# Optimization experiments

Measured on AMD Instinct MI355X. Metric: run time of the kernel, lower is better.

The kernel has to match this reference:

```python
import jax, jax.numpy as jnp
import numpy as np

N_NODES = 50000
N_EDGES = 600000
D = 128
EPS = 1e-5
AVG_D_LOG = float(np.log(4 + 1))  # avg_d={'log': log(avg_d+1)}, avg_d=4


def setup_inputs() -> dict:
    key = jax.random.key(0)
    ks = jax.random.split(key, 8)
    h = jax.random.normal(ks[0], (N_NODES, D), dtype=jnp.float32)
    # guarantee every node has at least one incoming edge (self-loop)
    edge_dst = jnp.concatenate([
        jnp.arange(N_NODES, dtype=jnp.int64),
        jax.random.randint(ks[1], (N_EDGES - N_NODES,), 0, N_NODES).astype(jnp.int64),
    ])
    edge_src = jax.random.randint(ks[2], (N_EDGES,), 0, N_NODES).astype(jnp.int64)
    def lin(k, fan_in, fan_out):
        lim = 1.0 / np.sqrt(fan_in)
        return jax.random.uniform(k, (fan_in, fan_out), jnp.float32, -lim, lim)
    W_pre = lin(ks[3], 2 * D, D)
    b_pre = jnp.zeros((D,), jnp.float32)
    W_post = lin(ks[4], 12 * D + D, D)  # 4 aggregators * 3 scalers * D + in_dim
    b_post = jnp.zeros((D,), jnp.float32)
    W_mix = lin(ks[5], D, D)
    b_mix = jnp.zeros((D,), jnp.float32)
    return {"h": h, "edge_src": edge_src, "edge_dst": edge_dst,
            "W_pre": W_pre, "b_pre": b_pre, "W_post": W_post,
            "b_post": b_post, "W_mix": W_mix, "b_mix": b_mix}


def reference(h, edge_src, edge_dst, W_pre, b_pre, W_post, b_post, W_mix, b_mix):
    n = h.shape[0]
    # pretrans_edges: cat(src, dst) -> Linear -> ReLU (MLP act) -> ReLU (outer)
    z2 = jnp.concatenate([h[edge_src], h[edge_dst]], axis=1)        # [E, 2D]
    e = jax.nn.relu(z2 @ W_pre + b_pre)                             # [E, D]
    # multi-aggregator segment reduce over destination nodes
    deg = jax.ops.segment_sum(jnp.ones_like(edge_dst, jnp.float32), edge_dst, n)  # [N]
    inv_deg = 1.0 / deg[:, None]
    mean = jax.ops.segment_sum(e, edge_dst, n) * inv_deg
    mean_sq = jax.ops.segment_sum(e * e, edge_dst, n) * inv_deg
    std = jnp.sqrt(jax.nn.relu(mean_sq - mean * mean) + EPS)
    mx = jax.ops.segment_max(e, edge_dst, n)
    mn = jax.ops.segment_min(e, edge_dst, n)
    agg = jnp.concatenate([mean, mx, mn, std], axis=1)              # [N, 4D]
    # scalers: identity, amplification, attenuation
    log_d = jnp.log(deg + 1.0)[:, None]
    scaled = jnp.concatenate([agg, agg * (log_d / AVG_D_LOG), agg * (AVG_D_LOG / log_d)], axis=1)  # [N, 12D]
    # posttrans: cat(h, aggregated) -> Linear -> ReLU
    hp = jax.nn.relu(jnp.concatenate([h, scaled], axis=1) @ W_post + b_post)  # [N, D]
    # mixing network + residual (node_dim == out_dim)
    out = h + jax.nn.leaky_relu(hp @ W_mix + b_mix, negative_slope=0.01)
    return out
```

## Files before the change

### kernel.cpp

```cpp
#include <hip/hip_runtime.h>
#include <hip/hip_bf16.h>

#define N_NODES 50000
#define N_EDGES 600000
#define D 128

constexpr float AVG_D_LOG = 1.6094379124341003f;
constexpr float EPS_V = 1e-5f;

#define PQ_B     0ul
#define AGG_B    25600000ul
#define HBF_B    76800000ul
#define WPRET2_B 89600000ul
#define WPOSTT_B 89665536ul
#define WMIXT_B  90091520ul
#define DEGC_B   90124288ul
#define OFF_B    90324288ul
#define CUR_B    90524352ul
#define SRCS_B   90724352ul
#define GCNT_B   93124352ul

typedef __attribute__((ext_vector_type(8))) short bf16x8;
typedef __attribute__((ext_vector_type(4))) float f32x4;

__device__ __forceinline__ short f2b(float f) {
    unsigned u = __builtin_bit_cast(unsigned, f);
    u += 0x7fffu + ((u >> 16) & 1u);
    return (short)(u >> 16);
}
__device__ __forceinline__ unsigned pk2(float a, float b) {
    return (unsigned)(unsigned short)f2b(a) | ((unsigned)(unsigned short)f2b(b) << 16);
}
__device__ __forceinline__ float blo(unsigned u) { return __uint_as_float(u << 16); }
__device__ __forceinline__ float bhi(unsigned u) { return __uint_as_float(u & 0xffff0000u); }

__device__ __forceinline__ void gld_lds16(const void* g, void* l) {
    __builtin_amdgcn_global_load_lds(
        (const __attribute__((address_space(1))) void*)g,
        (__attribute__((address_space(3))) void*)l, 16, 0, 0);
}

#define WAIT_BAR(N) do {                                              \
    asm volatile("s_waitcnt vmcnt(" #N ")" ::: "memory");             \
    __builtin_amdgcn_sched_barrier(0);                                \
    __builtin_amdgcn_s_barrier();                                     \
    __builtin_amdgcn_sched_barrier(0);                                \
} while (0)
#define BAR_ONLY() do {                                               \
    __builtin_amdgcn_sched_barrier(0);                                \
    __builtin_amdgcn_s_barrier();                                     \
    __builtin_amdgcn_sched_barrier(0);                                \
} while (0)

__global__ __launch_bounds__(256) void prep_kernel(
    const float* __restrict__ h, const float* __restrict__ Wpre,
    const float* __restrict__ Wpost, const float* __restrict__ Wmix,
    short* __restrict__ hbf, short* __restrict__ wpreT2,
    short* __restrict__ wpostT, short* __restrict__ wmixT,
    int* __restrict__ degc, int* __restrict__ cursor, int* __restrict__ gcnt)
{
    long i = (long)blockIdx.x * 256 + threadIdx.x;
    if (i < 800000) {
        float4 a = *(const float4*)(h + i * 8);
        float4 b = *(const float4*)(h + i * 8 + 4);
        int4 v;
        v.x = (int)pk2(a.x, a.y); v.y = (int)pk2(a.z, a.w);
        v.z = (int)pk2(b.x, b.y); v.w = (int)pk2(b.z, b.w);
        *(int4*)(hbf + i * 8) = v;
        return;
    }
    i -= 800000;
    if (i < 32768) {
        int n = i >> 7, k = i & 127;
        float v = (n < 128) ? Wpre[k * 128 + n] : Wpre[(k + 128) * 128 + (n - 128)];
        wpreT2[n * 128 + k] = f2b(v);
        return;
    }
    i -= 32768;
    if (i < 212992) { int k = i >> 7, n = i & 127; wpostT[n * 1664 + k] = f2b(Wpost[k * 128 + n]); return; }
    i -= 212992;
    if (i < 16384) { int k = i >> 7, n = i & 127; wmixT[n * 128 + k] = f2b(Wmix[k * 128 + n]); return; }
    i -= 16384;
    if (i < N_NODES) { degc[i] = 0; return; }
    i -= N_NODES;
    if (i < N_NODES) { cursor[i] = 0; return; }
    i -= N_NODES;
    if (i == 0) *gcnt = 0;
}
#define PREP_BLOCKS ((800000 + 32768 + 212992 + 16384 + 2 * N_NODES + 1 + 255) / 256)

__global__ __launch_bounds__(256) void hist_kernel(const int* __restrict__ edst, int* __restrict__ degc) {
    int e = blockIdx.x * 256 + threadIdx.x;
    if (e < N_EDGES) atomicAdd(&degc[edst[e]], 1);
}

__global__ __launch_bounds__(256) void alloc_kernel(const int* __restrict__ degc,
                                                    int* __restrict__ off, int* __restrict__ gcnt) {
    int n = blockIdx.x * 256 + threadIdx.x;
    int d = (n < N_NODES) ? degc[n] : 0;
    int pre = d;
#pragma unroll
    for (int o = 1; o < 64; o <<= 1) {
        int t = __shfl_up(pre, o);
        if ((threadIdx.x & 63) >= o) pre += t;
    }
    int base = 0;
    if ((threadIdx.x & 63) == 63) base = atomicAdd(gcnt, pre);
    base = __shfl(base, 63);
    if (n < N_NODES) off[n] = base + pre - d;
}

__global__ __launch_bounds__(256) void scatter_kernel(const int* __restrict__ esrc, const int* __restrict__ edst,
                                                      const int* __restrict__ off, int* __restrict__ cursor,
                                                      int* __restrict__ srcs) {
    int e = blockIdx.x * 256 + threadIdx.x;
    if (e < N_EDGES) {
        int d = edst[e];
        int p = off[d] + atomicAdd(&cursor[d], 1);
        srcs[p] = esrc[e];
    }
}

__device__ __forceinline__ void stageA_t(short* ldsT, const short* src, int rs, int co,
                                         int bn, int wv, int lane) {
    const int sub = lane >> 3, seg = lane & 7;
    const int sg = (seg ^ sub) * 8;
#pragma unroll
    for (int t = 0; t < 4; t++) {
        int i = wv * 4 + t;
        int row = i * 8 + sub;
        int n = bn + row; if (n >= N_NODES) n = N_NODES - 1;
        gld_lds16(src + (long)n * rs + co + sg, ldsT + i * 512);
    }
}
__device__ __forceinline__ void stageB_t(short* ldsT, const short* src, int rs, int co,
                                         int wv, int lane) {
    const int sub = lane >> 3, seg = lane & 7;
    const int sg = (seg ^ sub) * 8;
#pragma unroll
    for (int t = 0; t < 4; t++) {
        int i = wv * 4 + t;
        int row = i * 8 + sub;
        gld_lds16(src + (long)row * rs + co + sg, ldsT + i * 512);
    }
}

#define MFMA_ITER(AB, BB, ACC)                                                      \
    {                                                                               \
        _Pragma("unroll")                                                           \
        for (int ks = 0; ks < 2; ks++) {                                            \
            const int qx = (((ks * 4 + quad) ^ r7) * 8);                            \
            bf16x8 a0 = *(const bf16x8*)&(AB)[(wv * 32 + lm) * 64 + qx];            \
            bf16x8 a1 = *(const bf16x8*)&(AB)[(wv * 32 + 16 + lm) * 64 + qx];       \
            _Pragma("unroll")                                                       \
            for (int ct = 0; ct < 8; ct++) {                                        \
                bf16x8 b = *(const bf16x8*)&(BB)[(ct * 16 + lm) * 64 + qx];         \
                ACC[0][ct] = __builtin_amdgcn_mfma_f32_16x16x32_bf16(b, a0, ACC[0][ct], 0, 0, 0); \
                ACC[1][ct] = __builtin_amdgcn_mfma_f32_16x16x32_bf16(b, a1, ACC[1][ct], 0, 0, 0); \
            }                                                                       \
        }                                                                           \
    }

__global__ __launch_bounds__(256, 2) void gemm_pq_kernel(
    const short* __restrict__ hbf, const short* __restrict__ wpreT2,
    const float* __restrict__ bpre, short* __restrict__ PQ)
{
    __shared__ __align__(16) short As[2][8192];
    __shared__ __align__(16) short Bs[2][8192];

    const int tid = threadIdx.x;
    const int cg = blockIdx.x & 1;
    const int bn = (blockIdx.x >> 1) * 128;
    const int lane = tid & 63, wv = tid >> 6;
    const int lm = lane & 15, quad = lane >> 4;
    const int r7 = lm & 7;
    const short* Bsrc = wpreT2 + cg * 128 * 128;

    f32x4 acc[2][8];
#pragma unroll
    for (int a = 0; a < 2; a++)
#pragma unroll
        for (int b = 0; b < 8; b++) acc[a][b] = (f32x4){0.f, 0.f, 0.f, 0.f};

    stageA_t(As[0], hbf, 128, 0, bn, wv, lane);
    stageB_t(Bs[0], Bsrc, 128, 0, wv, lane);
    stageA_t(As[1], hbf, 128, 64, bn, wv, lane);
    stageB_t(Bs[1], Bsrc, 128, 64, wv, lane);
    WAIT_BAR(8);
    MFMA_ITER(As[0], Bs[0], acc);
    WAIT_BAR(0);
    MFMA_ITER(As[1], Bs[1], acc);

#pragma unroll
    for (int rt = 0; rt < 2; rt++) {
        int row = wv * 32 + rt * 16 + lm;
        int n = bn + row;
        if (n >= N_NODES) continue;
        short* dst = PQ + (long)n * 256;
#pragma unroll
        for (int ct = 0; ct < 8; ct++) {
            int col = cg * 128 + ct * 16 + quad * 4;
            float v0 = acc[rt][ct][0], v1 = acc[rt][ct][1], v2 = acc[rt][ct][2], v3 = acc[rt][ct][3];
            if (cg) {
                float4 bv = *(const float4*)(bpre + (col - 128));
                v0 += bv.x; v1 += bv.y; v2 += bv.z; v3 += bv.w;
            }
            int2 pkd; pkd.x = (int)pk2(v0, v1); pkd.y = (int)pk2(v2, v3);
            *(int2*)(dst + col) = pkd;
        }
    }
}

__global__ __launch_bounds__(256) void edgestats_kernel(
    const short* __restrict__ PQ, const int* __restrict__ srcs,
    const int* __restrict__ off, const int* __restrict__ degc, short* __restrict__ aggbf)
{
    const int wv = threadIdx.x >> 6, lane = threadIdx.x & 63;
    const int n = blockIdx.x * 4 + wv;
    const unsigned* Pb = (const unsigned*)PQ;

    const int s0 = __builtin_amdgcn_readfirstlane(off[n]);
    const int s1 = s0 + __builtin_amdgcn_readfirstlane(degc[n]);

    unsigned qu = Pb[(long)n * 128 + 64 + lane];
    const float qa = blo(qu), qb = bhi(qu);

    float sA = 0.f, sB = 0.f, qA = 0.f, qB = 0.f;
    float mxA = -1e30f, mxB = -1e30f, mnA = 1e30f, mnB = 1e30f;

    int p = s0;
    for (; p + 8 <= s1; p += 8) {
        int idx[8];
#pragma unroll
        for (int j = 0; j < 8; j++) idx[j] = srcs[p + j];
        unsigned u[8];
#pragma unroll
        for (int j = 0; j < 8; j++) u[j] = Pb[(long)idx[j] * 128 + lane];
#pragma unroll
        for (int j = 0; j < 8; j++) {
            float a = blo(u[j]) + qa; a = a > 0.f ? a : 0.f;
            float b = bhi(u[j]) + qb; b = b > 0.f ? b : 0.f;
            sA += a; sB += b; qA += a * a; qB += b * b;
            mxA = fmaxf(mxA, a); mxB = fmaxf(mxB, b);
            mnA = fminf(mnA, a); mnB = fminf(mnB, b);
        }
    }
    if (p + 4 <= s1) {
        int idx[4];
#pragma unroll
        for (int j = 0; j < 4; j++) idx[j] = srcs[p + j];
        unsigned u[4];
#pragma unroll
        for (int j = 0; j < 4; j++) u[j] = Pb[(long)idx[j] * 128 + lane];
#pragma unroll
        for (int j = 0; j < 4; j++) {
            float a = blo(u[j]) + qa; a = a > 0.f ? a : 0.f;
            float b = bhi(u[j]) + qb; b = b > 0.f ? b : 0.f;
            sA += a; sB += b; qA += a * a; qB += b * b;
            mxA = fmaxf(mxA, a); mxB = fmaxf(mxB, b);
            mnA = fminf(mnA, a); mnB = fminf(mnB, b);
        }
        p += 4;
    }
    for (; p < s1; p++) {
        unsigned u = Pb[(long)srcs[p] * 128 + lane];
        float a = blo(u) + qa; a = a > 0.f ? a : 0.f;
        float b = bhi(u) + qb; b = b > 0.f ? b : 0.f;
        sA += a; sB += b; qA += a * a; qB += b * b;
        mxA = fmaxf(mxA, a); mxB = fmaxf(mxB, b);
        mnA = fminf(mnA, a); mnB = fminf(mnB, b);
    }

    float inv = 1.0f / (float)(s1 - s0);
    float mA = sA * inv, mB = sB * inv;
    float vA = qA * inv - mA * mA; vA = vA > 0.f ? vA : 0.f;
    float vB = qB * inv - mB * mB; vB = vB > 0.f ? vB : 0.f;
    float stA = sqrtf(vA + EPS_V), stB = sqrtf(vB + EPS_V);

    unsigned* ag = (unsigned*)(aggbf + (long)n * 512);
    ag[lane]       = pk2(mA, mB);
    ag[64 + lane]  = pk2(mxA, mxB);
    ag[128 + lane] = pk2(mnA, mnB);
    ag[192 + lane] = pk2(stA, stB);
}

__global__ __launch_bounds__(256, 2) void node_kernel(
    const float* __restrict__ h, const short* __restrict__ hbf, const short* __restrict__ aggbf,
    const int* __restrict__ degc, const short* __restrict__ wpostT, const float* __restrict__ bpost,
    const short* __restrict__ wmixT, const float* __restrict__ bmix, float* __restrict__ out)
{
    __shared__ __align__(16) short As[2][8192];
    __shared__ __align__(16) short Bs[2][8192];
    __shared__ float sAmp[128], sAtt[128];

    const int tid = threadIdx.x;
    const int bn = blockIdx.x * 128;
    const int lane = tid & 63, wv = tid >> 6;
    const int lm = lane & 15, quad = lane >> 4;
    const int r7 = lm & 7;

    if (tid < 128) {
        int n = bn + tid; if (n >= N_NODES) n = N_NODES - 1;
        float d = (float)degc[n];
        float ld = logf(d + 1.0f);
        sAmp[tid] = ld * (1.0f / AVG_D_LOG);
        sAtt[tid] = AVG_D_LOG / ld;
    }
    __syncthreads();

    f32x4 accI[2][8], accM[2][8], accT[2][8];
#pragma unroll
    for (int a = 0; a < 2; a++)
#pragma unroll
        for (int b = 0; b < 8; b++) {
            accI[a][b] = (f32x4){0.f, 0.f, 0.f, 0.f};
            accM[a][b] = (f32x4){0.f, 0.f, 0.f, 0.f};
            accT[a][b] = (f32x4){0.f, 0.f, 0.f, 0.f};
        }


    stageA_t(As[0], hbf, 128, 0, bn, wv, lane);
    stageB_t(Bs[0], wpostT, 1664, 0, wv, lane);

    stageA_t(As[1], hbf, 128, 64, bn, wv, lane);
    stageB_t(Bs[1], wpostT, 1664, 64, wv, lane);
    WAIT_BAR(8);
    MFMA_ITER(As[0], Bs[0], accI);
    BAR_ONLY();

    stageB_t(Bs[0], wpostT, 1664, 2 * 64, wv, lane);
    stageA_t(As[0], aggbf, 512, 0, bn, wv, lane);
    WAIT_BAR(8);
    MFMA_ITER(As[1], Bs[1], accI);
    BAR_ONLY();

    int pb = 0;
    for (int j = 0; j < 8; j++) {
        const short* Ac = As[j & 1];
        stageB_t(Bs[pb ^ 1], wpostT, 1664, (10 + j) * 64, wv, lane);
        if (j < 7) {
            int jn = j + 1;
            stageA_t(As[jn & 1], aggbf, 512, (jn >> 1) * 128 + (jn & 1) * 64, bn, wv, lane);
            WAIT_BAR(8);
        } else {
            WAIT_BAR(4);
        }
        MFMA_ITER(Ac, Bs[pb], accI);
        BAR_ONLY();

        stageB_t(Bs[pb], wpostT, 1664, (18 + j) * 64, wv, lane);
        if (j < 7) { WAIT_BAR(8); } else { WAIT_BAR(4); }
        MFMA_ITER(Ac, Bs[pb ^ 1], accM);
        BAR_ONLY();

        if (j < 7) stageB_t(Bs[pb ^ 1], wpostT, 1664, (3 + j) * 64, wv, lane);
        else       stageB_t(Bs[pb ^ 1], wmixT, 128, 0, wv, lane);
        WAIT_BAR(4);
        MFMA_ITER(Ac, Bs[pb], accT);
        BAR_ONLY();
        pb ^= 1;
    }

    stageB_t(Bs[1], wmixT, 128, 64, wv, lane);

    const float am0 = sAmp[wv * 32 + lm],      at0 = sAtt[wv * 32 + lm];
    const float am1 = sAmp[wv * 32 + 16 + lm], at1 = sAtt[wv * 32 + 16 + lm];
#pragma unroll
    for (int rt = 0; rt < 2; rt++) {
        const float am = rt ? am1 : am0, at = rt ? at1 : at0;
        const int row = wv * 32 + rt * 16 + lm;
#pragma unroll
        for (int ct = 0; ct < 8; ct++) {
            float4 bv = *(const float4*)(bpost + ct * 16 + quad * 4);
            float v0 = accI[rt][ct][0] + am * accM[rt][ct][0] + at * accT[rt][ct][0] + bv.x;
            float v1 = accI[rt][ct][1] + am * accM[rt][ct][1] + at * accT[rt][ct][1] + bv.y;
            float v2 = accI[rt][ct][2] + am * accM[rt][ct][2] + at * accT[rt][ct][2] + bv.z;
            float v3 = accI[rt][ct][3] + am * accM[rt][ct][3] + at * accT[rt][ct][3] + bv.w;
            v0 = v0 > 0.f ? v0 : 0.f; v1 = v1 > 0.f ? v1 : 0.f;
            v2 = v2 > 0.f ? v2 : 0.f; v3 = v3 > 0.f ? v3 : 0.f;
            int2 pkd; pkd.x = (int)pk2(v0, v1); pkd.y = (int)pk2(v2, v3);
            const int cb = (ct & 3) * 32 + quad * 8;
            const int sb = ((((cb >> 4) ^ r7) << 4) | (cb & 15));
            *(int2*)((char*)As[ct >> 2] + row * 128 + sb) = pkd;
        }
    }
    __syncthreads();

    f32x4 accO[2][8];
#pragma unroll
    for (int a = 0; a < 2; a++)
#pragma unroll
        for (int b = 0; b < 8; b++) accO[a][b] = (f32x4){0.f, 0.f, 0.f, 0.f};
#pragma unroll
    for (int kc = 0; kc < 2; kc++) {
        MFMA_ITER(As[kc], Bs[kc], accO);
    }

#pragma unroll
    for (int rt = 0; rt < 2; rt++) {
        int row = wv * 32 + rt * 16 + lm;
        int n = bn + row;
        if (n >= N_NODES) continue;
#pragma unroll
        for (int ct = 0; ct < 8; ct++) {
            int col = ct * 16 + quad * 4;
            float4 bv = *(const float4*)(bmix + col);
            float4 hv = *(const float4*)(h + (long)n * 128 + col);
            float4 o;
            float v0 = accO[rt][ct][0] + bv.x; v0 = v0 > 0.f ? v0 : 0.01f * v0; o.x = hv.x + v0;
            float v1 = accO[rt][ct][1] + bv.y; v1 = v1 > 0.f ? v1 : 0.01f * v1; o.y = hv.y + v1;
            float v2 = accO[rt][ct][2] + bv.z; v2 = v2 > 0.f ? v2 : 0.01f * v2; o.z = hv.z + v2;
            float v3 = accO[rt][ct][3] + bv.w; v3 = v3 > 0.f ? v3 : 0.01f * v3; o.w = hv.w + v3;
            *(float4*)(out + (long)n * 128 + col) = o;
        }
    }
}

extern "C" void kernel_launch(void* const* d_in, const int* in_sizes, int n_in,
                              void* d_out, int out_size, void* d_ws, size_t ws_size,
                              hipStream_t stream) {
    const float* h     = (const float*)d_in[0];
    const int*   esrc  = (const int*)d_in[1];
    const int*   edst  = (const int*)d_in[2];
    const float* Wpre  = (const float*)d_in[3];
    const float* bpre  = (const float*)d_in[4];
    const float* Wpost = (const float*)d_in[5];
    const float* bpost = (const float*)d_in[6];
    const float* Wmix  = (const float*)d_in[7];
    const float* bmix  = (const float*)d_in[8];
    float* out = (float*)d_out;
    char* ws = (char*)d_ws;

    short* PQ     = (short*)(ws + PQ_B);
    short* aggbf  = (short*)(ws + AGG_B);
    short* hbf    = (short*)(ws + HBF_B);
    short* wpreT2 = (short*)(ws + WPRET2_B);
    short* wpostT = (short*)(ws + WPOSTT_B);
    short* wmixT  = (short*)(ws + WMIXT_B);
    int*   degc   = (int*)(ws + DEGC_B);
    int*   off    = (int*)(ws + OFF_B);
    int*   cursor = (int*)(ws + CUR_B);
    int*   srcs   = (int*)(ws + SRCS_B);
    int*   gcnt   = (int*)(ws + GCNT_B);

    prep_kernel<<<PREP_BLOCKS, 256, 0, stream>>>(h, Wpre, Wpost, Wmix, hbf, wpreT2, wpostT, wmixT, degc, cursor, gcnt);
    hist_kernel<<<(N_EDGES + 255) / 256, 256, 0, stream>>>(edst, degc);
    alloc_kernel<<<(N_NODES + 255) / 256, 256, 0, stream>>>(degc, off, gcnt);
    scatter_kernel<<<(N_EDGES + 255) / 256, 256, 0, stream>>>(esrc, edst, off, cursor, srcs);
    gemm_pq_kernel<<<((N_NODES + 127) / 128) * 2, 256, 0, stream>>>(hbf, wpreT2, bpre, PQ);
    edgestats_kernel<<<N_NODES / 4, 256, 0, stream>>>(PQ, srcs, off, degc, aggbf);
    node_kernel<<<(N_NODES + 127) / 128, 256, 0, stream>>>(h, hbf, aggbf, degc, wpostT, bpost, wmixT, bmix, out);
}
```

Measured before the change: 254.5 us.

## Fold scaler accumulators into one and load A fragments into registers in post GEMM

```diff
diff --git a/kernel.cpp b/kernel.cpp
--- a/kernel.cpp
+++ b/kernel.cpp
@@ -51,6 +51,7 @@
     __builtin_amdgcn_s_barrier();                                     \
     __builtin_amdgcn_sched_barrier(0);                                \
 } while (0)
+#define SB0() __builtin_amdgcn_sched_barrier(0)
 
 __global__ __launch_bounds__(256) void prep_kernel(
     const float* __restrict__ h, const float* __restrict__ Wpre,
@@ -144,6 +145,16 @@
         gld_lds16(src + (long)row * rs + co + sg, ldsT + i * 512);
     }
 }
+__device__ __forceinline__ void loadAfr(bf16x8* a, const short* src, int rs, int co,
+                                        int bn, int wv, int lm, int quad) {
+#pragma unroll
+    for (int rt = 0; rt < 2; rt++)
+#pragma unroll
+        for (int ks = 0; ks < 2; ks++) {
+            int n = bn + wv * 32 + rt * 16 + lm; if (n >= N_NODES) n = N_NODES - 1;
+            a[rt * 2 + ks] = *(const bf16x8*)(src + (long)n * rs + co + ks * 32 + quad * 8);
+        }
+}
 
 #define MFMA_ITER(AB, BB, ACC)                                                      \
     {                                                                               \
@@ -161,6 +172,24 @@
         }                                                                           \
     }
 
+#define MFMA_RG(BB, AF, ACC, FRESH)                                                 \
+    {                                                                               \
+        __builtin_amdgcn_s_setprio(1);                                              \
+        _Pragma("unroll")                                                           \
+        for (int ks = 0; ks < 2; ks++) {                                            \
+            const int qx = ((ks * 4 + quad) ^ r7) * 8;                              \
+            _Pragma("unroll")                                                       \
+            for (int ct = 0; ct < 8; ct++) {                                        \
+                bf16x8 b = *(const bf16x8*)&(BB)[(ct * 16 + lm) * 64 + qx];         \
+                f32x4 c0 = ((FRESH) && ks == 0) ? (f32x4){0.f, 0.f, 0.f, 0.f} : ACC[0][ct]; \
+                f32x4 c1 = ((FRESH) && ks == 0) ? (f32x4){0.f, 0.f, 0.f, 0.f} : ACC[1][ct]; \
+                ACC[0][ct] = __builtin_amdgcn_mfma_f32_16x16x32_bf16(b, (AF)[ks], c0, 0, 0, 0); \
+                ACC[1][ct] = __builtin_amdgcn_mfma_f32_16x16x32_bf16(b, (AF)[2 + ks], c1, 0, 0, 0); \
+            }                                                                       \
+        }                                                                           \
+        __builtin_amdgcn_s_setprio(0);                                              \
+    }
+
 __global__ __launch_bounds__(256, 2) void gemm_pq_kernel(
     const short* __restrict__ hbf, const short* __restrict__ wpreT2,
     const float* __restrict__ bpre, short* __restrict__ PQ)
@@ -308,76 +337,88 @@
     }
     __syncthreads();
 
-    f32x4 accI[2][8], accM[2][8], accT[2][8];
-#pragma unroll
-    for (int a = 0; a < 2; a++)
-#pragma unroll
-        for (int b = 0; b < 8; b++) {
-            accI[a][b] = (f32x4){0.f, 0.f, 0.f, 0.f};
-            accM[a][b] = (f32x4){0.f, 0.f, 0.f, 0.f};
-            accT[a][b] = (f32x4){0.f, 0.f, 0.f, 0.f};
-        }
-
-
-    stageA_t(As[0], hbf, 128, 0, bn, wv, lane);
+    const float am0 = sAmp[wv * 32 + lm],      at0 = sAtt[wv * 32 + lm];
+    const float am1 = sAmp[wv * 32 + 16 + lm], at1 = sAtt[wv * 32 + 16 + lm];
+
+    f32x4 mI[2][8];
+
+    bf16x8 hA0[4], hA1[4];
+    loadAfr(hA0, hbf, 128, 0, bn, wv, lm, quad);
+    SB0();
     stageB_t(Bs[0], wpostT, 1664, 0, wv, lane);
-
-    stageA_t(As[1], hbf, 128, 64, bn, wv, lane);
+    SB0();
+    loadAfr(hA1, hbf, 128, 64, bn, wv, lm, quad);
+    SB0();
+    stageA_t(As[0], aggbf, 512, 0, bn, wv, lane);
+
+    WAIT_BAR(8);
     stageB_t(Bs[1], wpostT, 1664, 64, wv, lane);
-    WAIT_BAR(8);
-    MFMA_ITER(As[0], Bs[0], accI);
-    BAR_ONLY();
-
+    SB0();
+    stageA_t(As[1], aggbf, 512, 64, bn, wv, lane);
+    MFMA_RG(Bs[0], hA0, mI, 1);
+
+    WAIT_BAR(4);
     stageB_t(Bs[0], wpostT, 1664, 2 * 64, wv, lane);
-    stageA_t(As[0], aggbf, 512, 0, bn, wv, lane);
-    WAIT_BAR(8);
-    MFMA_ITER(As[1], Bs[1], accI);
-    BAR_ONLY();
-
-    int pb = 0;
+    MFMA_RG(Bs[1], hA1, mI, 0);
+
     for (int j = 0; j < 8; j++) {
-        const short* Ac = As[j & 1];
-        stageB_t(Bs[pb ^ 1], wpostT, 1664, (10 + j) * 64, wv, lane);
+        const int pb = j & 1, pn = pb ^ 1;
+        const short* Ac = As[pb];
+        bf16x8 aR[4];
+
+        WAIT_BAR(0);
+        stageB_t(Bs[pn], wpostT, 1664, (10 + j) * 64, wv, lane);
+#pragma unroll
+        for (int rt = 0; rt < 2; rt++)
+#pragma unroll
+            for (int ks = 0; ks < 2; ks++)
+                aR[rt * 2 + ks] = *(const bf16x8*)&Ac[(wv * 32 + rt * 16 + lm) * 64 + ((ks * 4 + quad) ^ r7) * 8];
+        MFMA_RG(Bs[pb], aR, mI, 0);
+
+        WAIT_BAR(0);
+        stageB_t(Bs[pb], wpostT, 1664, (18 + j) * 64, wv, lane);
+        SB0();
         if (j < 7) {
             int jn = j + 1;
-            stageA_t(As[jn & 1], aggbf, 512, (jn >> 1) * 128 + (jn & 1) * 64, bn, wv, lane);
-            WAIT_BAR(8);
-        } else {
-            WAIT_BAR(4);
-        }
-        MFMA_ITER(Ac, Bs[pb], accI);
-        BAR_ONLY();
-
-        stageB_t(Bs[pb], wpostT, 1664, (18 + j) * 64, wv, lane);
-        if (j < 7) { WAIT_BAR(8); } else { WAIT_BAR(4); }
-        MFMA_ITER(Ac, Bs[pb ^ 1], accM);
-        BAR_ONLY();
-
-        if (j < 7) stageB_t(Bs[pb ^ 1], wpostT, 1664, (3 + j) * 64, wv, lane);
-        else       stageB_t(Bs[pb ^ 1], wmixT, 128, 0, wv, lane);
-        WAIT_BAR(4);
-        MFMA_ITER(Ac, Bs[pb], accT);
-        BAR_ONLY();
-        pb ^= 1;
-    }
-
+            stageA_t(As[pn], aggbf, 512, (jn >> 1) * 128 + (jn & 1) * 64, bn, wv, lane);
+        }
+        {
+            f32x4 tp[2][8];
+            MFMA_RG(Bs[pn], aR, tp, 1);
+#pragma unroll
+            for (int ct = 0; ct < 8; ct++) {
+                mI[0][ct] += am0 * tp[0][ct];
+                mI[1][ct] += am1 * tp[1][ct];
+            }
+        }
+
+        if (j < 7) { WAIT_BAR(4); } else { WAIT_BAR(0); }
+        if (j < 7) stageB_t(Bs[pn], wpostT, 1664, (3 + j) * 64, wv, lane);
+        else       stageB_t(Bs[pn], wmixT, 128, 0, wv, lane);
+        {
+            f32x4 tp[2][8];
+            MFMA_RG(Bs[pb], aR, tp, 1);
+#pragma unroll
+            for (int ct = 0; ct < 8; ct++) {
+                mI[0][ct] += at0 * tp[0][ct];
+                mI[1][ct] += at1 * tp[1][ct];
+            }
+        }
+    }
+
+    BAR_ONLY();
     stageB_t(Bs[1], wmixT, 128, 64, wv, lane);
 
-    const float am0 = sAmp[wv * 32 + lm],      at0 = sAtt[wv * 32 + lm];
-    const float am1 = sAmp[wv * 32 + 16 + lm], at1 = sAtt[wv * 32 + 16 + lm];
 #pragma unroll
     for (int rt = 0; rt < 2; rt++) {
-        const float am = rt ? am1 : am0, at = rt ? at1 : at0;
         const int row = wv * 32 + rt * 16 + lm;
 #pragma unroll
         for (int ct = 0; ct < 8; ct++) {
             float4 bv = *(const float4*)(bpost + ct * 16 + quad * 4);
-            float v0 = accI[rt][ct][0] + am * accM[rt][ct][0] + at * accT[rt][ct][0] + bv.x;
-            float v1 = accI[rt][ct][1] + am * accM[rt][ct][1] + at * accT[rt][ct][1] + bv.y;
-            float v2 = accI[rt][ct][2] + am * accM[rt][ct][2] + at * accT[rt][ct][2] + bv.z;
-            float v3 = accI[rt][ct][3] + am * accM[rt][ct][3] + at * accT[rt][ct][3] + bv.w;
-            v0 = v0 > 0.f ? v0 : 0.f; v1 = v1 > 0.f ? v1 : 0.f;
-            v2 = v2 > 0.f ? v2 : 0.f; v3 = v3 > 0.f ? v3 : 0.f;
+            float v0 = mI[rt][ct][0] + bv.x; v0 = v0 > 0.f ? v0 : 0.f;
+            float v1 = mI[rt][ct][1] + bv.y; v1 = v1 > 0.f ? v1 : 0.f;
+            float v2 = mI[rt][ct][2] + bv.z; v2 = v2 > 0.f ? v2 : 0.f;
+            float v3 = mI[rt][ct][3] + bv.w; v3 = v3 > 0.f ? v3 : 0.f;
             int2 pkd; pkd.x = (int)pk2(v0, v1); pkd.y = (int)pk2(v2, v3);
             const int cb = (ct & 3) * 32 + quad * 8;
             const int sb = ((((cb >> 4) ^ r7) << 4) | (cb & 15));
```

Measured after the change: 244.4 us. -4.0%, faster.
